# Kernel optimization log

Hardware: AMD Instinct MI355X
Metric: run time of the kernel (lower is better)

Reference implementation:

```python
import jax, jax.numpy as jnp
import numpy as np

ALPHA = 1.0
GAMMA = 2.0
SMOOTH = 1e-07
B, S = 8192, 4096


def setup_inputs() -> dict:
    key = jax.random.key(0)
    k1, k2, k3, k4 = jax.random.split(key, 4)
    scores = jax.random.normal(k1, (B, S), dtype=jnp.float32)
    head_position = jax.random.randint(k2, (B,), 0, S, dtype=jnp.int64) if jax.config.jax_enable_x64 else jax.random.randint(k2, (B,), 0, S).astype(jnp.int32)
    tail_position = jax.random.randint(k3, (B,), 0, S).astype(head_position.dtype)
    score_mask = jax.random.randint(k4, (B, S), 0, 2, dtype=jnp.int32)
    return {"scores": scores, "head_position": head_position,
            "tail_position": tail_position, "score_mask": score_mask}


def reference(scores, head_position, tail_position, score_mask):
    # scores: [B, S] float; head/tail_position: [B] int; score_mask: [B, S] int
    batch_size = scores.shape[0]
    bidx = jnp.arange(batch_size)
    # exclude head and tail positions from the negative set
    m = score_mask.at[bidx, head_position].set(-1)
    m = m.at[bidx, tail_position].set(-1)
    neg = (m == 1)  # [B, S] candidate negatives
    # positive score per sample, broadcast against all candidates
    pos = jnp.take_along_axis(scores, tail_position[:, None], axis=1)  # [B, 1]
    # log_softmax over the pair [pos, neg_j] at index 0 == -softplus(neg - pos)
    logpt = -jax.nn.softplus(scores - pos)  # [B, S]
    pt = jnp.clip(jnp.exp(logpt), SMOOTH, 1.0 - SMOOTH)
    fl = -ALPHA * jnp.power(1.0 - pt, GAMMA) * logpt  # [B, S] per-pair focal loss
    negf = neg.astype(scores.dtype)
    cnt = negf.sum(axis=1)  # [B] number of negatives
    # per-sample focal_loss is the MEAN over its pairs; samples with 0 negs skipped
    per_sample = jnp.where(cnt > 0, (fl * negf).sum(axis=1) / jnp.maximum(cnt, 1.0), 0.0)
    return per_sample.sum() / batch_size
```

## Files before the change

### kernel.cpp

```cpp
#include <hip/hip_runtime.h>


template <int S>
__global__ __launch_bounds__(256, 8) void focal_row_kernel(
    const float* __restrict__ scores,
    const int*   __restrict__ head_pos,
    const int*   __restrict__ tail_pos,
    const int*   __restrict__ mask,
    float*       __restrict__ row_out,
    int B)
{
    const int lane = threadIdx.x & 63;
    const int row  = blockIdx.x * 4 + (threadIdx.x >> 6);
    if (row >= B) return;

    const int head = head_pos[row];
    const int tail = tail_pos[row];
    const float4* s4 = reinterpret_cast<const float4*>(scores + (size_t)row * S);
    const int4*   m4 = reinterpret_cast<const int4*>(mask   + (size_t)row * S);
    const float pos = scores[(size_t)row * S + tail];

    float fsum = 0.f;
    int   cnt  = 0;

    constexpr int NV4 = S / 4 / 64;
    static_assert(NV4 % 4 == 0, "S must be divisible by 1024");
    #pragma unroll
    for (int g = 0; g < NV4 / 4; ++g) {
        float4 sv[4]; int4 mv[4];
        #pragma unroll
        for (int u = 0; u < 4; ++u) {
            const int v = lane + 64 * (4 * g + u);
            sv[u] = s4[v];
            mv[u] = m4[v];
        }
        #pragma unroll
        for (int u = 0; u < 4; ++u) {
            const int base = (lane + 64 * (4 * g + u)) << 2;
            const float se[4] = {sv[u].x, sv[u].y, sv[u].z, sv[u].w};
            const int   me[4] = {mv[u].x, mv[u].y, mv[u].z, mv[u].w};
            #pragma unroll
            for (int k = 0; k < 4; ++k) {
                const int idx = base + k;
                const float x  = se[k] - pos;
                const float e  = __expf(x);
                const float t  = 1.f + e;
                const float sp = __logf(t);
                float pt = __builtin_amdgcn_rcpf(t);
                pt = fminf(fmaxf(pt, 1e-7f), 1.f - 1e-7f);
                const float om = 1.f - pt;
                const float fl = om * om * sp;
                const bool isneg = (me[k] == 1) & (idx != head) & (idx != tail);
                if (isneg) { fsum += fl; cnt += 1; }
            }
        }
    }

    #pragma unroll
    for (int off = 32; off; off >>= 1) {
        fsum += __shfl_down(fsum, off, 64);
        cnt  += __shfl_down(cnt,  off, 64);
    }
    if (lane == 0)
        row_out[row] = (cnt > 0) ? fsum / (float)cnt : 0.f;
}

__global__ __launch_bounds__(256) void focal_row_generic(
    const float* __restrict__ scores,
    const int*   __restrict__ head_pos,
    const int*   __restrict__ tail_pos,
    const int*   __restrict__ mask,
    float*       __restrict__ row_out,
    int S)
{
    const int row  = blockIdx.x;
    const int tid  = threadIdx.x;
    const int head = head_pos[row];
    const int tail = tail_pos[row];
    const float* srow = scores + (size_t)row * S;
    const int*   mrow = mask   + (size_t)row * S;
    const float pos = srow[tail];
    float fsum = 0.f; int cnt = 0;
    for (int idx = tid; idx < S; idx += 256) {
        const float x  = srow[idx] - pos;
        const float e  = __expf(x);
        const float t  = 1.f + e;
        const float sp = __logf(t);
        float pt = __builtin_amdgcn_rcpf(t);
        pt = fminf(fmaxf(pt, 1e-7f), 1.f - 1e-7f);
        const float om = 1.f - pt;
        const float fl = om * om * sp;
        if ((mrow[idx] == 1) && (idx != head) && (idx != tail)) { fsum += fl; cnt += 1; }
    }
    #pragma unroll
    for (int off = 32; off; off >>= 1) {
        fsum += __shfl_down(fsum, off, 64);
        cnt  += __shfl_down(cnt,  off, 64);
    }
    __shared__ float sf[4]; __shared__ int sc[4];
    const int wave = tid >> 6;
    if ((tid & 63) == 0) { sf[wave] = fsum; sc[wave] = cnt; }
    __syncthreads();
    if (tid == 0) {
        float tot = sf[0] + sf[1] + sf[2] + sf[3];
        int   c   = sc[0] + sc[1] + sc[2] + sc[3];
        row_out[row] = (c > 0) ? tot / (float)c : 0.f;
    }
}

__global__ __launch_bounds__(256) void final_reduce_kernel(
    const float* __restrict__ row_out, float* __restrict__ out, int B)
{
    float sum = 0.f;
    const float4* r4 = reinterpret_cast<const float4*>(row_out);
    const int nvec = B >> 2;
    for (int i = threadIdx.x; i < nvec; i += 256) {
        float4 v = r4[i];
        sum += (v.x + v.y) + (v.z + v.w);
    }
    #pragma unroll
    for (int off = 32; off; off >>= 1) sum += __shfl_down(sum, off, 64);
    __shared__ float sf[4];
    const int wave = threadIdx.x >> 6;
    if ((threadIdx.x & 63) == 0) sf[wave] = sum;
    __syncthreads();
    if (threadIdx.x == 0) out[0] = (sf[0] + sf[1] + sf[2] + sf[3]) / (float)B;
}

extern "C" void kernel_launch(void* const* d_in, const int* in_sizes, int n_in,
                              void* d_out, int out_size, void* d_ws, size_t ws_size,
                              hipStream_t stream)
{
    const float* scores = (const float*)d_in[0];
    const int*   headp  = (const int*)d_in[1];
    const int*   tailp  = (const int*)d_in[2];
    const int*   maskp  = (const int*)d_in[3];
    const int B = in_sizes[1];
    const int S = in_sizes[0] / B;

    float* rowbuf = (float*)d_ws;
    float* out    = (float*)d_out;

    if (S == 4096) {
        const int grid = (B + 3) / 4;
        focal_row_kernel<4096><<<grid, 256, 0, stream>>>(scores, headp, tailp, maskp, rowbuf, B);
    } else {
        focal_row_generic<<<B, 256, 0, stream>>>(scores, headp, tailp, maskp, rowbuf, S);
    }
    final_reduce_kernel<<<1, 256, 0, stream>>>(rowbuf, out, B);
}
```

Baseline: 283.4 us.

## Software-pipeline row loads and move head/tail exclusion out of inner loop

Replaces the grouped load-then-compute loop with a rolling register prefetch of depth four, so the loads for later iterations are in flight while the current vector is being computed. Drops the per-element head/tail index comparisons and instead has lane 0 subtract those terms afterwards. Also turns the masked accumulation into branch-free multiply-adds with a float counter. Float accumulation of the count and the subtract-afterwards correction can differ slightly in rounding from the original. The loop is memory-bound, so the benefit depends on whether the compiler already overlapped the loads.

```diff
diff --git a/kernel.cpp b/kernel.cpp
--- a/kernel.cpp
+++ b/kernel.cpp
@@ -1,5 +1,15 @@
 #include <hip/hip_runtime.h>
 
+
+__device__ __forceinline__ float focal_term(float x) {
+    const float e  = __expf(x);
+    const float t  = 1.f + e;
+    const float sp = __logf(t);
+    float pt = __builtin_amdgcn_rcpf(t);
+    pt = fminf(fmaxf(pt, 1e-7f), 1.f - 1e-7f);
+    const float om = 1.f - pt;
+    return om * om * sp;
+}
 
 template <int S>
 __global__ __launch_bounds__(256, 8) void focal_row_kernel(
@@ -16,43 +26,43 @@
 
     const int head = head_pos[row];
     const int tail = tail_pos[row];
-    const float4* s4 = reinterpret_cast<const float4*>(scores + (size_t)row * S);
-    const int4*   m4 = reinterpret_cast<const int4*>(mask   + (size_t)row * S);
-    const float pos = scores[(size_t)row * S + tail];
+    const float* srow = scores + (size_t)row * S;
+    const int*   mrow = mask   + (size_t)row * S;
+    const float4* s4 = reinterpret_cast<const float4*>(srow);
+    const int4*   m4 = reinterpret_cast<const int4*>(mrow);
+    const float pos = srow[tail];
+
+    constexpr int NIT   = S / 4 / 64;
+    constexpr int DEPTH = 4;
+    static_assert(NIT >= DEPTH && NIT % 4 == 0, "shape");
+
+    float4 sbuf[DEPTH];
+    int4   mbuf[DEPTH];
+    #pragma unroll
+    for (int i = 0; i < DEPTH; ++i) {
+        sbuf[i] = s4[lane + 64 * i];
+        mbuf[i] = m4[lane + 64 * i];
+    }
 
     float fsum = 0.f;
-    int   cnt  = 0;
+    float cnt  = 0.f;
 
-    constexpr int NV4 = S / 4 / 64;
-    static_assert(NV4 % 4 == 0, "S must be divisible by 1024");
     #pragma unroll
-    for (int g = 0; g < NV4 / 4; ++g) {
-        float4 sv[4]; int4 mv[4];
+    for (int i = 0; i < NIT; ++i) {
+        const float4 sv = sbuf[i & (DEPTH - 1)];
+        const int4   mv = mbuf[i & (DEPTH - 1)];
+        if (i + DEPTH < NIT) {
+            sbuf[i & (DEPTH - 1)] = s4[lane + 64 * (i + DEPTH)];
+            mbuf[i & (DEPTH - 1)] = m4[lane + 64 * (i + DEPTH)];
+        }
+        const float se[4] = {sv.x, sv.y, sv.z, sv.w};
+        const int   me[4] = {mv.x, mv.y, mv.z, mv.w};
         #pragma unroll
-        for (int u = 0; u < 4; ++u) {
-            const int v = lane + 64 * (4 * g + u);
-            sv[u] = s4[v];
-            mv[u] = m4[v];
-        }
-        #pragma unroll
-        for (int u = 0; u < 4; ++u) {
-            const int base = (lane + 64 * (4 * g + u)) << 2;
-            const float se[4] = {sv[u].x, sv[u].y, sv[u].z, sv[u].w};
-            const int   me[4] = {mv[u].x, mv[u].y, mv[u].z, mv[u].w};
-            #pragma unroll
-            for (int k = 0; k < 4; ++k) {
-                const int idx = base + k;
-                const float x  = se[k] - pos;
-                const float e  = __expf(x);
-                const float t  = 1.f + e;
-                const float sp = __logf(t);
-                float pt = __builtin_amdgcn_rcpf(t);
-                pt = fminf(fmaxf(pt, 1e-7f), 1.f - 1e-7f);
-                const float om = 1.f - pt;
-                const float fl = om * om * sp;
-                const bool isneg = (me[k] == 1) & (idx != head) & (idx != tail);
-                if (isneg) { fsum += fl; cnt += 1; }
-            }
+        for (int k = 0; k < 4; ++k) {
+            const float fl = focal_term(se[k] - pos);
+            const float on = (me[k] == 1) ? 1.f : 0.f;
+            fsum += fl * on;
+            cnt  += on;
         }
     }
 
@@ -61,8 +71,12 @@
         fsum += __shfl_down(fsum, off, 64);
         cnt  += __shfl_down(cnt,  off, 64);
     }
-    if (lane == 0)
-        row_out[row] = (cnt > 0) ? fsum / (float)cnt : 0.f;
+
+    if (lane == 0) {
+        if (mrow[head] == 1) { fsum -= focal_term(srow[head] - pos); cnt -= 1.f; }
+        if (tail != head && mrow[tail] == 1) { fsum -= focal_term(0.f); cnt -= 1.f; }
+        row_out[row] = (cnt > 0.f) ? fsum / cnt : 0.f;
+    }
 }
 
 __global__ __launch_bounds__(256) void focal_row_generic(
@@ -80,31 +94,25 @@
     const float* srow = scores + (size_t)row * S;
     const int*   mrow = mask   + (size_t)row * S;
     const float pos = srow[tail];
-    float fsum = 0.f; int cnt = 0;
+    float fsum = 0.f; float cnt = 0.f;
     for (int idx = tid; idx < S; idx += 256) {
-        const float x  = srow[idx] - pos;
-        const float e  = __expf(x);
-        const float t  = 1.f + e;
-        const float sp = __logf(t);
-        float pt = __builtin_amdgcn_rcpf(t);
-        pt = fminf(fmaxf(pt, 1e-7f), 1.f - 1e-7f);
-        const float om = 1.f - pt;
-        const float fl = om * om * sp;
-        if ((mrow[idx] == 1) && (idx != head) && (idx != tail)) { fsum += fl; cnt += 1; }
+        const float fl = focal_term(srow[idx] - pos);
+        const bool isneg = (mrow[idx] == 1) && (idx != head) && (idx != tail);
+        if (isneg) { fsum += fl; cnt += 1.f; }
     }
     #pragma unroll
     for (int off = 32; off; off >>= 1) {
         fsum += __shfl_down(fsum, off, 64);
         cnt  += __shfl_down(cnt,  off, 64);
     }
-    __shared__ float sf[4]; __shared__ int sc[4];
+    __shared__ float sf[4]; __shared__ float sc[4];
     const int wave = tid >> 6;
     if ((tid & 63) == 0) { sf[wave] = fsum; sc[wave] = cnt; }
     __syncthreads();
     if (tid == 0) {
         float tot = sf[0] + sf[1] + sf[2] + sf[3];
-        int   c   = sc[0] + sc[1] + sc[2] + sc[3];
-        row_out[row] = (c > 0) ? tot / (float)c : 0.f;
+        float c   = sc[0] + sc[1] + sc[2] + sc[3];
+        row_out[row] = (c > 0.f) ? tot / c : 0.f;
     }
 }
 
```

After: 288.2 us. No clear change (+1.7%).
